# Kernel optimization log

Hardware: AMD Instinct MI355X
Metric: run time of the kernel (lower is better)

Reference implementation:

```python
import jax, jax.numpy as jnp
import numpy as np

EMBED_DIM = 1024
NUM_HEADS = 16
HEAD_DIM = EMBED_DIM // NUM_HEADS
BATCH = 2
SEQ = 2048


def setup_inputs() -> dict:
    key = jax.random.key(0)
    ks = jax.random.split(key, 10)
    s = 1.0 / np.sqrt(EMBED_DIM)
    inp = {
        "query": jax.random.normal(ks[0], (BATCH, SEQ, EMBED_DIM), jnp.float32),
        # Linear weights stored as [in, out] (y = x @ W + b)
        "wq": jax.random.normal(ks[1], (EMBED_DIM, EMBED_DIM), jnp.float32) * s,
        "bq": jnp.zeros((EMBED_DIM,), jnp.float32),
        "wk": jax.random.normal(ks[2], (EMBED_DIM, EMBED_DIM), jnp.float32) * s,
        "bk": jnp.zeros((EMBED_DIM,), jnp.float32),
        "wv": jax.random.normal(ks[3], (EMBED_DIM, EMBED_DIM), jnp.float32) * s,
        "bv": jnp.zeros((EMBED_DIM,), jnp.float32),
        "wo": jax.random.normal(ks[4], (EMBED_DIM, EMBED_DIM), jnp.float32) * s,
        "bo": jnp.zeros((EMBED_DIM,), jnp.float32),
        "temperature": jnp.float32(HEAD_DIM),  # learnable temperature, init = head_dim
    }
    return inp


def reference(query, wq, bq, wk, bk, wv, bv, wo, bo, temperature):
    B, S, E = query.shape
    # self-attention: key = value = query
    Q = (query @ wq + bq).reshape(B, S, NUM_HEADS, HEAD_DIM).transpose(0, 2, 1, 3)
    K = (query @ wk + bk).reshape(B, S, NUM_HEADS, HEAD_DIM).transpose(0, 2, 1, 3)
    V = (query @ wv + bv).reshape(B, S, NUM_HEADS, HEAD_DIM).transpose(0, 2, 1, 3)
    # squared Euclidean distances: ||q||^2 + ||k||^2 - 2<q,k>
    q_sq = jnp.sum(Q * Q, axis=-1, keepdims=True)          # (B,H,Sq,1)
    k_sq = jnp.sum(K * K, axis=-1, keepdims=True)          # (B,H,Sk,1)
    qk = jnp.einsum("bhqd,bhkd->bhqk", Q, K)
    d_sq = jnp.maximum(q_sq + jnp.swapaxes(k_sq, -2, -1) - 2.0 * qk, 0.0)
    attn = jax.nn.softmax(-d_sq / temperature, axis=-1)    # (B,H,Sq,Sk)
    out = jnp.einsum("bhqk,bhkd->bhqd", attn, V)
    out = out.transpose(0, 2, 1, 3).reshape(B, S, E)
    return out @ wo + bo
```

## Files before the change

kernel.cpp:

```cpp
#include <hip/hip_runtime.h>
#include <stdint.h>
#include <stddef.h>


#define LOG2E 1.44269504088896f

typedef __attribute__((ext_vector_type(8))) short bf16x8;
typedef __attribute__((ext_vector_type(4))) float f32x4;
typedef __attribute__((ext_vector_type(4))) unsigned short u16x4;
typedef __attribute__((ext_vector_type(8))) unsigned short u16x8;

__device__ __forceinline__ unsigned short f2b(float f) {
  union { float f; unsigned int u; } x; x.f = f;
  unsigned int u = x.u;
  u += 0x7fffu + ((u >> 16) & 1u);
  return (unsigned short)(u >> 16);
}
__device__ __forceinline__ float b2f(unsigned short s) {
  union { unsigned int u; float f; } x; x.u = ((unsigned int)s) << 16;
  return x.f;
}

#define GLD_LDS(g, l) __builtin_amdgcn_global_load_lds( \
    (const __attribute__((address_space(1))) void*)(g), \
    (__attribute__((address_space(3))) void*)(l), 16, 0, 0)

__global__ void convx_kernel(const float* __restrict__ X, unsigned short* __restrict__ Xb) {
  int i = (blockIdx.x * 256 + threadIdx.x) * 4;
  f32x4 v = *(const f32x4*)&X[i];
  u16x4 o;
  #pragma unroll
  for (int j = 0; j < 4; ++j) o[j] = f2b(v[j]);
  *(u16x4*)&Xb[i] = o;
}

__global__ void transw_kernel(const float* __restrict__ wq, const float* __restrict__ wk,
                              const float* __restrict__ wv, const float* __restrict__ wo,
                              unsigned short* __restrict__ WTqkv, unsigned short* __restrict__ WTo) {
  __shared__ float tile[64][65];
  int z = blockIdx.z;
  const float* src = (z == 0) ? wq : (z == 1) ? wk : (z == 2) ? wv : wo;
  unsigned short* dst = (z < 3) ? (WTqkv + (size_t)z * 1024 * 1024) : WTo;
  int k0 = blockIdx.y * 64, n0 = blockIdx.x * 64;
  int rr = threadIdx.x >> 6, cc = threadIdx.x & 63;
  #pragma unroll
  for (int p = 0; p < 16; ++p) {
    int row = p * 4 + rr;
    tile[row][cc] = src[(size_t)(k0 + row) * 1024 + n0 + cc];
  }
  __syncthreads();
  #pragma unroll
  for (int p = 0; p < 16; ++p) {
    int row = p * 4 + rr;
    dst[(size_t)(n0 + row) * 1024 + k0 + cc] = f2b(tile[cc][row]);
  }
}

__global__ __launch_bounds__(256, 2) void gemm_qkv_kernel(
    const unsigned short* __restrict__ X, const unsigned short* __restrict__ WT,
    const float* __restrict__ bq, const float* __restrict__ bk, const float* __restrict__ bv,
    unsigned short* __restrict__ Qb, unsigned short* __restrict__ Kb,
    unsigned short* __restrict__ VTo) {
  __shared__ unsigned short As[2 * 128 * 32];
  __shared__ unsigned short Bs[2 * 128 * 32];
  const int t = threadIdx.x, w = t >> 6, lane = t & 63;
  const int r = lane & 15, q4 = lane >> 4;
  const int m0 = blockIdx.y * 128, n0 = blockIdx.x * 128;
  const int wr = (w >> 1) * 64, wc = (w & 1) * 64;
  const unsigned short* Xg = X + (size_t)m0 * 1024;
  const unsigned short* Wg = WT + (size_t)n0 * 1024;
  f32x4 acc[4][4] = {};
  for (int k0 = 0; k0 < 1024; k0 += 64) {
    #pragma unroll
    for (int g = 0; g < 4; ++g) {
      int slot = g * 256 + t;
      int kh = slot >> 9, row = (slot >> 2) & 127, ko = (slot & 3) * 8;
      GLD_LDS(Xg + (size_t)row * 1024 + k0 + kh * 32 + ko, &As[(g * 256 + w * 64) * 8]);
      GLD_LDS(Wg + (size_t)row * 1024 + k0 + kh * 32 + ko, &Bs[(g * 256 + w * 64) * 8]);
    }
    __syncthreads();
    #pragma unroll
    for (int kh = 0; kh < 2; ++kh) {
      bf16x8 af[4], bfr[4];
      #pragma unroll
      for (int mf = 0; mf < 4; ++mf)
        af[mf] = *(const bf16x8*)&As[kh * 4096 + (wr + mf * 16 + r) * 32 + q4 * 8];
      #pragma unroll
      for (int nf = 0; nf < 4; ++nf)
        bfr[nf] = *(const bf16x8*)&Bs[kh * 4096 + (wc + nf * 16 + r) * 32 + q4 * 8];
      #pragma unroll
      for (int mf = 0; mf < 4; ++mf)
        #pragma unroll
        for (int nf = 0; nf < 4; ++nf)
          acc[mf][nf] = __builtin_amdgcn_mfma_f32_16x16x32_bf16(af[mf], bfr[nf], acc[mf][nf], 0, 0, 0);
    }
    __syncthreads();
  }
  const int nblk = n0 >> 10;
  if (nblk < 2) {
    const float* bias = (nblk == 0) ? bq : bk;
    unsigned short* OutB = (nblk == 0) ? Qb : Kb;
    const int nc0 = n0 & 1023;
    #pragma unroll
    for (int nf = 0; nf < 4; ++nf) {
      int n = nc0 + wc + nf * 16 + r;
      float bb = bias[n];
      #pragma unroll
      for (int mf = 0; mf < 4; ++mf) {
        int m = m0 + wr + mf * 16 + q4 * 4;
        f32x4 v = acc[mf][nf];
        #pragma unroll
        for (int i = 0; i < 4; ++i)
          OutB[(size_t)(m + i) * 1024 + n] = f2b(v[i] + bb);
      }
    }
  } else {
    const int c0 = n0 - 2048;
    #pragma unroll
    for (int nf = 0; nf < 4; ++nf) {
      int c = c0 + wc + nf * 16 + r;
      float bb = bv[c];
      int h = c >> 6, d = c & 63;
      #pragma unroll
      for (int mf = 0; mf < 4; ++mf) {
        int m = m0 + wr + mf * 16 + q4 * 4;
        int b = m >> 11, s = m & 2047;
        f32x4 v = acc[mf][nf];
        u16x4 pk;
        #pragma unroll
        for (int i = 0; i < 4; ++i) pk[i] = f2b(v[i] + bb);
        *(u16x4*)&VTo[((size_t)((b * 16 + h) * 64 + d)) * 2048 + s] = pk;
      }
    }
  }
}

__global__ void sumsq_kernel(const unsigned short* __restrict__ Qb,
                             const unsigned short* __restrict__ Kb,
                             const float* __restrict__ temp,
                             float* __restrict__ qs2, float* __restrict__ ks2) {
  int idx = blockIdx.x * 256 + threadIdx.x;
  int bh = idx >> 11, s = idx & 2047;
  int b = bh >> 4, h = bh & 15;
  const u16x8* qp = (const u16x8*)(Qb + (size_t)(b * 2048 + s) * 1024 + h * 64);
  const u16x8* kp = (const u16x8*)(Kb + (size_t)(b * 2048 + s) * 1024 + h * 64);
  float scale = LOG2E / temp[0];
  float sq = 0.f, sk = 0.f;
  #pragma unroll
  for (int c = 0; c < 8; ++c) {
    u16x8 vq = qp[c], vk = kp[c];
    #pragma unroll
    for (int j = 0; j < 8; ++j) {
      float q = b2f(vq[j]); sq += q * q;
      float k = b2f(vk[j]); sk += k * k;
    }
  }
  qs2[idx] = sq * scale;
  ks2[idx] = sk * scale;
}

__global__ __launch_bounds__(256, 2) void flash_kernel(
    const unsigned short* __restrict__ Qb, const unsigned short* __restrict__ Kb,
    const unsigned short* __restrict__ VT, const float* __restrict__ qs2,
    const float* __restrict__ ks2, const float* __restrict__ temp,
    unsigned short* __restrict__ AO) {
  __shared__ unsigned short Ks[2][2 * 64 * 32];
  __shared__ unsigned short Vs[2][2 * 64 * 32];
  __shared__ unsigned short Ps[4][32 * 68];
  const int t = threadIdx.x, w = t >> 6, lane = t & 63;
  const int r = lane & 15, q4 = lane >> 4;
  const int bh = blockIdx.y, b = bh >> 4, h = bh & 15;
  const int q0 = blockIdx.x * 128;
  const float cc = 2.0f * LOG2E / temp[0];

  bf16x8 qf[2][2];
  #pragma unroll
  for (int mf = 0; mf < 2; ++mf) {
    int sq = q0 + w * 32 + mf * 16 + r;
    const unsigned short* qp = Qb + (size_t)(b * 2048 + sq) * 1024 + h * 64;
    #pragma unroll
    for (int ks = 0; ks < 2; ++ks) qf[mf][ks] = *(const bf16x8*)(qp + ks * 32 + q4 * 8);
  }
  f32x4 qsv[2];
  #pragma unroll
  for (int mf = 0; mf < 2; ++mf)
    qsv[mf] = *(const f32x4*)&qs2[bh * 2048 + q0 + w * 32 + mf * 16 + q4 * 4];

  f32x4 accO[2][4] = {};
  f32x4 lsum[2] = {};
  bf16x8 ones;
  #pragma unroll
  for (int j = 0; j < 8; ++j) ones[j] = (short)0x3F80;

  const unsigned short* Kg = Kb + ((size_t)b * 2048) * 1024 + h * 64;
  const unsigned short* Vg = VT + ((size_t)bh * 64) * 2048;
  const float* kqb = ks2 + bh * 2048 + r;

  #pragma unroll
  for (int g = 0; g < 2; ++g) {
    int slot = g * 256 + t;
    int half = slot >> 8, key = (slot >> 2) & 63, ko = (slot & 3) * 8;
    GLD_LDS(Kg + (size_t)key * 1024 + half * 32 + ko, &Ks[0][(g * 256 + w * 64) * 8]);
    GLD_LDS(Vg + (size_t)key * 2048 + half * 32 + ko, &Vs[0][(g * 256 + w * 64) * 8]);
  }
  float kq[4];
  #pragma unroll
  for (int nf = 0; nf < 4; ++nf) kq[nf] = kqb[nf * 16];

  #pragma unroll 2
  for (int c = 0; c < 32; ++c) {
    const int buf = c & 1;
    __syncthreads();
    float kqn[4];
    if (c < 31) {
      #pragma unroll
      for (int g = 0; g < 2; ++g) {
        int slot = g * 256 + t;
        int half = slot >> 8, key = (slot >> 2) & 63, ko = (slot & 3) * 8;
        GLD_LDS(Kg + (size_t)((c + 1) * 64 + key) * 1024 + half * 32 + ko,
                &Ks[buf ^ 1][(g * 256 + w * 64) * 8]);
        GLD_LDS(Vg + (size_t)key * 2048 + (c + 1) * 64 + half * 32 + ko,
                &Vs[buf ^ 1][(g * 256 + w * 64) * 8]);
      }
      #pragma unroll
      for (int nf = 0; nf < 4; ++nf) kqn[nf] = kqb[(c + 1) * 64 + nf * 16];
    }

    f32x4 accS[2][4] = {};
    #pragma unroll
    for (int ks = 0; ks < 2; ++ks) {
      #pragma unroll
      for (int nf = 0; nf < 4; ++nf) {
        bf16x8 kf = *(const bf16x8*)&Ks[buf][(ks * 64 + nf * 16 + r) * 32 + q4 * 8];
        accS[0][nf] = __builtin_amdgcn_mfma_f32_16x16x32_bf16(qf[0][ks], kf, accS[0][nf], 0, 0, 0);
        accS[1][nf] = __builtin_amdgcn_mfma_f32_16x16x32_bf16(qf[1][ks], kf, accS[1][nf], 0, 0, 0);
      }
    }
    #pragma unroll
    for (int mf = 0; mf < 2; ++mf) {
      #pragma unroll
      for (int nf = 0; nf < 4; ++nf) {
        #pragma unroll
        for (int i = 0; i < 4; ++i) {
          float u = __builtin_fmaf(cc, accS[mf][nf][i], -kq[nf] - qsv[mf][i]);
          float p = __builtin_amdgcn_exp2f(fminf(u, 0.f));
          union { float f; unsigned int u; } pu; pu.f = p;
          Ps[w][(mf * 16 + q4 * 4 + i) * 68 + nf * 16 + r] = (unsigned short)(pu.u >> 16);
        }
      }
    }
    #pragma unroll
    for (int ks = 0; ks < 2; ++ks) {
      bf16x8 vb[4];
      #pragma unroll
      for (int df = 0; df < 4; ++df)
        vb[df] = *(const bf16x8*)&Vs[buf][(ks * 64 + df * 16 + r) * 32 + q4 * 8];
      #pragma unroll
      for (int mf = 0; mf < 2; ++mf) {
        bf16x8 pa = *(const bf16x8*)&Ps[w][(mf * 16 + r) * 68 + ks * 32 + q4 * 8];
        lsum[mf] = __builtin_amdgcn_mfma_f32_16x16x32_bf16(pa, ones, lsum[mf], 0, 0, 0);
        #pragma unroll
        for (int df = 0; df < 4; ++df)
          accO[mf][df] = __builtin_amdgcn_mfma_f32_16x16x32_bf16(pa, vb[df], accO[mf][df], 0, 0, 0);
      }
    }
    if (c < 31) {
      #pragma unroll
      for (int nf = 0; nf < 4; ++nf) kq[nf] = kqn[nf];
    }
  }
  #pragma unroll
  for (int mf = 0; mf < 2; ++mf) {
    float inv[4];
    #pragma unroll
    for (int i = 0; i < 4; ++i) inv[i] = 1.0f / lsum[mf][i];
    #pragma unroll
    for (int df = 0; df < 4; ++df) {
      int d = df * 16 + r;
      #pragma unroll
      for (int i = 0; i < 4; ++i) {
        int sq = q0 + w * 32 + mf * 16 + q4 * 4 + i;
        AO[(size_t)(b * 2048 + sq) * 1024 + h * 64 + d] = f2b(accO[mf][df][i] * inv[i]);
      }
    }
  }
}

__global__ __launch_bounds__(256, 2) void gemm_out_kernel(
    const unsigned short* __restrict__ A, const unsigned short* __restrict__ WT,
    const float* __restrict__ bo, float* __restrict__ Out) {
  __shared__ unsigned short As[2 * 128 * 32];
  __shared__ unsigned short Bs[2 * 64 * 32];
  const int t = threadIdx.x, w = t >> 6, lane = t & 63;
  const int r = lane & 15, q4 = lane >> 4;
  const int m0 = blockIdx.y * 128, n0 = blockIdx.x * 64;
  const int wr = (w >> 1) * 64, wc = (w & 1) * 32;
  const unsigned short* Ag = A + (size_t)m0 * 1024;
  const unsigned short* Wg = WT + (size_t)n0 * 1024;
  f32x4 acc[4][2] = {};
  for (int k0 = 0; k0 < 1024; k0 += 64) {
    #pragma unroll
    for (int g = 0; g < 4; ++g) {
      int slot = g * 256 + t;
      int kh = slot >> 9, row = (slot >> 2) & 127, ko = (slot & 3) * 8;
      GLD_LDS(Ag + (size_t)row * 1024 + k0 + kh * 32 + ko, &As[(g * 256 + w * 64) * 8]);
    }
    #pragma unroll
    for (int g = 0; g < 2; ++g) {
      int slot = g * 256 + t;
      int kh = slot >> 8, row = (slot >> 2) & 63, ko = (slot & 3) * 8;
      GLD_LDS(Wg + (size_t)row * 1024 + k0 + kh * 32 + ko, &Bs[(g * 256 + w * 64) * 8]);
    }
    __syncthreads();
    #pragma unroll
    for (int kh = 0; kh < 2; ++kh) {
      bf16x8 af[4], bfr[2];
      #pragma unroll
      for (int mf = 0; mf < 4; ++mf)
        af[mf] = *(const bf16x8*)&As[kh * 4096 + (wr + mf * 16 + r) * 32 + q4 * 8];
      #pragma unroll
      for (int nf = 0; nf < 2; ++nf)
        bfr[nf] = *(const bf16x8*)&Bs[kh * 2048 + (wc + nf * 16 + r) * 32 + q4 * 8];
      #pragma unroll
      for (int mf = 0; mf < 4; ++mf)
        #pragma unroll
        for (int nf = 0; nf < 2; ++nf)
          acc[mf][nf] = __builtin_amdgcn_mfma_f32_16x16x32_bf16(af[mf], bfr[nf], acc[mf][nf], 0, 0, 0);
    }
    __syncthreads();
  }
  #pragma unroll
  for (int nf = 0; nf < 2; ++nf) {
    int n = n0 + wc + nf * 16 + r;
    float bb = bo[n];
    #pragma unroll
    for (int mf = 0; mf < 4; ++mf) {
      int m = m0 + wr + mf * 16 + q4 * 4;
      f32x4 v = acc[mf][nf];
      #pragma unroll
      for (int i = 0; i < 4; ++i)
        Out[(size_t)(m + i) * 1024 + n] = v[i] + bb;
    }
  }
}

extern "C" void kernel_launch(void* const* d_in, const int* in_sizes, int n_in,
                              void* d_out, int out_size, void* d_ws, size_t ws_size,
                              hipStream_t stream) {
  const float* X    = (const float*)d_in[0];
  const float* wq   = (const float*)d_in[1];
  const float* bq   = (const float*)d_in[2];
  const float* wk   = (const float*)d_in[3];
  const float* bk   = (const float*)d_in[4];
  const float* wv   = (const float*)d_in[5];
  const float* bv   = (const float*)d_in[6];
  const float* wo   = (const float*)d_in[7];
  const float* bo   = (const float*)d_in[8];
  const float* temp = (const float*)d_in[9];
  float* Out = (float*)d_out;

  char* ws = (char*)d_ws;
  unsigned short* Xb    = (unsigned short*)ws; ws += (size_t)4096 * 1024 * 2;
  unsigned short* WTqkv = (unsigned short*)ws; ws += (size_t)3072 * 1024 * 2;
  unsigned short* WTo   = (unsigned short*)ws; ws += (size_t)1024 * 1024 * 2;
  unsigned short* Qb    = (unsigned short*)ws; ws += (size_t)4096 * 1024 * 2;
  unsigned short* Kb    = (unsigned short*)ws; ws += (size_t)4096 * 1024 * 2;
  unsigned short* VT    = (unsigned short*)ws; ws += (size_t)4096 * 1024 * 2;
  unsigned short* AO    = (unsigned short*)ws; ws += (size_t)4096 * 1024 * 2;
  float* qs2 = (float*)ws; ws += (size_t)65536 * 4;
  float* ks2 = (float*)ws; ws += (size_t)65536 * 4;

  convx_kernel<<<4096, 256, 0, stream>>>(X, Xb);
  transw_kernel<<<dim3(16, 16, 4), 256, 0, stream>>>(wq, wk, wv, wo, WTqkv, WTo);
  gemm_qkv_kernel<<<dim3(24, 32), 256, 0, stream>>>(Xb, WTqkv, bq, bk, bv, Qb, Kb, VT);
  sumsq_kernel<<<256, 256, 0, stream>>>(Qb, Kb, temp, qs2, ks2);
  flash_kernel<<<dim3(16, 32), 256, 0, stream>>>(Qb, Kb, VT, qs2, ks2, temp, AO);
  gemm_out_kernel<<<dim3(16, 32), 256, 0, stream>>>(AO, WTo, bo, Out);
}
```

Measured before the change: 209.8 us.

## Fuse prep kernels, fold sum-of-squares into QKV GEMM, keep P in registers

Merges the X conversion and weight transpose into one launch, and computes the per-head squared norms of Q and K inside the QKV GEMM epilogue using shuffle reductions, which removes the separate sumsq kernel and its re-read of Q and K. The flash kernel now computes S transposed, so the exponentiated probabilities land directly in MFMA A-operand layout. This drops the LDS round trip through Ps. V tiles are stored in LDS with an XOR swizzle and read as two 4-element halves, and the QKV GEMM launch bounds are raised to 3 blocks per SM. The changes add epilogue work and register pressure in the GEMM in exchange for fewer launches and less memory traffic.

```diff
diff --git a/kernel.cpp b/kernel.cpp
--- a/kernel.cpp
+++ b/kernel.cpp
@@ -6,9 +6,9 @@
 #define LOG2E 1.44269504088896f
 
 typedef __attribute__((ext_vector_type(8))) short bf16x8;
+typedef __attribute__((ext_vector_type(4))) short bf16x4;
 typedef __attribute__((ext_vector_type(4))) float f32x4;
 typedef __attribute__((ext_vector_type(4))) unsigned short u16x4;
-typedef __attribute__((ext_vector_type(8))) unsigned short u16x8;
 
 __device__ __forceinline__ unsigned short f2b(float f) {
   union { float f; unsigned int u; } x; x.f = f;
@@ -20,25 +20,34 @@
   union { unsigned int u; float f; } x; x.u = ((unsigned int)s) << 16;
   return x.f;
 }
+__device__ __forceinline__ unsigned int fbits(float f) {
+  union { float f; unsigned int u; } x; x.f = f; return x.u;
+}
 
 #define GLD_LDS(g, l) __builtin_amdgcn_global_load_lds( \
     (const __attribute__((address_space(1))) void*)(g), \
     (__attribute__((address_space(3))) void*)(l), 16, 0, 0)
 
-__global__ void convx_kernel(const float* __restrict__ X, unsigned short* __restrict__ Xb) {
-  int i = (blockIdx.x * 256 + threadIdx.x) * 4;
-  f32x4 v = *(const f32x4*)&X[i];
-  u16x4 o;
-  #pragma unroll
-  for (int j = 0; j < 4; ++j) o[j] = f2b(v[j]);
-  *(u16x4*)&Xb[i] = o;
-}
-
-__global__ void transw_kernel(const float* __restrict__ wq, const float* __restrict__ wk,
-                              const float* __restrict__ wv, const float* __restrict__ wo,
-                              unsigned short* __restrict__ WTqkv, unsigned short* __restrict__ WTo) {
+__global__ void prep_kernel(const float* __restrict__ X,
+                            const float* __restrict__ wq, const float* __restrict__ wk,
+                            const float* __restrict__ wv, const float* __restrict__ wo,
+                            unsigned short* __restrict__ Xb,
+                            unsigned short* __restrict__ WTqkv, unsigned short* __restrict__ WTo) {
+  int z = blockIdx.z;
+  if (z == 4) {
+    size_t base = ((size_t)(blockIdx.y * 16 + blockIdx.x)) * 16384;
+    #pragma unroll
+    for (int j = 0; j < 16; ++j) {
+      size_t i = base + (size_t)(j * 256 + threadIdx.x) * 4;
+      f32x4 v = *(const f32x4*)&X[i];
+      u16x4 o;
+      #pragma unroll
+      for (int k = 0; k < 4; ++k) o[k] = f2b(v[k]);
+      *(u16x4*)&Xb[i] = o;
+    }
+    return;
+  }
   __shared__ float tile[64][65];
-  int z = blockIdx.z;
   const float* src = (z == 0) ? wq : (z == 1) ? wk : (z == 2) ? wv : wo;
   unsigned short* dst = (z < 3) ? (WTqkv + (size_t)z * 1024 * 1024) : WTo;
   int k0 = blockIdx.y * 64, n0 = blockIdx.x * 64;
@@ -56,11 +65,11 @@
   }
 }
 
-__global__ __launch_bounds__(256, 2) void gemm_qkv_kernel(
+__global__ __launch_bounds__(256, 3) void gemm_qkv_kernel(
     const unsigned short* __restrict__ X, const unsigned short* __restrict__ WT,
     const float* __restrict__ bq, const float* __restrict__ bk, const float* __restrict__ bv,
     unsigned short* __restrict__ Qb, unsigned short* __restrict__ Kb,
-    unsigned short* __restrict__ VTo) {
+    unsigned short* __restrict__ VTo, float* __restrict__ qs2, float* __restrict__ ks2) {
   __shared__ unsigned short As[2 * 128 * 32];
   __shared__ unsigned short Bs[2 * 128 * 32];
   const int t = threadIdx.x, w = t >> 6, lane = t & 63;
@@ -100,7 +109,9 @@
   if (nblk < 2) {
     const float* bias = (nblk == 0) ? bq : bk;
     unsigned short* OutB = (nblk == 0) ? Qb : Kb;
+    float* S2 = (nblk == 0) ? qs2 : ks2;
     const int nc0 = n0 & 1023;
+    float s2a[4][4] = {};
     #pragma unroll
     for (int nf = 0; nf < 4; ++nf) {
       int n = nc0 + wc + nf * 16 + r;
@@ -110,8 +121,34 @@
         int m = m0 + wr + mf * 16 + q4 * 4;
         f32x4 v = acc[mf][nf];
         #pragma unroll
+        for (int i = 0; i < 4; ++i) {
+          unsigned short os = f2b(v[i] + bb);
+          OutB[(size_t)(m + i) * 1024 + n] = os;
+          float xb = b2f(os);
+          s2a[mf][i] += xb * xb;
+        }
+      }
+    }
+    #pragma unroll
+    for (int mf = 0; mf < 4; ++mf)
+      #pragma unroll
+      for (int i = 0; i < 4; ++i) {
+        float v = s2a[mf][i];
+        v += __shfl_xor(v, 1, 64);
+        v += __shfl_xor(v, 2, 64);
+        v += __shfl_xor(v, 4, 64);
+        v += __shfl_xor(v, 8, 64);
+        s2a[mf][i] = v;
+      }
+    if (r == 0) {
+      int hh = (nc0 + wc) >> 6;
+      #pragma unroll
+      for (int mf = 0; mf < 4; ++mf) {
+        int m = m0 + wr + mf * 16 + q4 * 4;
+        int bb2 = m >> 11, ss = m & 2047;
+        #pragma unroll
         for (int i = 0; i < 4; ++i)
-          OutB[(size_t)(m + i) * 1024 + n] = f2b(v[i] + bb);
+          S2[(size_t)(bb2 * 16 + hh) * 2048 + ss + i] = s2a[mf][i];
       }
     }
   } else {
@@ -135,43 +172,19 @@
   }
 }
 
-__global__ void sumsq_kernel(const unsigned short* __restrict__ Qb,
-                             const unsigned short* __restrict__ Kb,
-                             const float* __restrict__ temp,
-                             float* __restrict__ qs2, float* __restrict__ ks2) {
-  int idx = blockIdx.x * 256 + threadIdx.x;
-  int bh = idx >> 11, s = idx & 2047;
-  int b = bh >> 4, h = bh & 15;
-  const u16x8* qp = (const u16x8*)(Qb + (size_t)(b * 2048 + s) * 1024 + h * 64);
-  const u16x8* kp = (const u16x8*)(Kb + (size_t)(b * 2048 + s) * 1024 + h * 64);
-  float scale = LOG2E / temp[0];
-  float sq = 0.f, sk = 0.f;
-  #pragma unroll
-  for (int c = 0; c < 8; ++c) {
-    u16x8 vq = qp[c], vk = kp[c];
-    #pragma unroll
-    for (int j = 0; j < 8; ++j) {
-      float q = b2f(vq[j]); sq += q * q;
-      float k = b2f(vk[j]); sk += k * k;
-    }
-  }
-  qs2[idx] = sq * scale;
-  ks2[idx] = sk * scale;
-}
-
 __global__ __launch_bounds__(256, 2) void flash_kernel(
     const unsigned short* __restrict__ Qb, const unsigned short* __restrict__ Kb,
     const unsigned short* __restrict__ VT, const float* __restrict__ qs2,
     const float* __restrict__ ks2, const float* __restrict__ temp,
     unsigned short* __restrict__ AO) {
-  __shared__ unsigned short Ks[2][2 * 64 * 32];
-  __shared__ unsigned short Vs[2][2 * 64 * 32];
-  __shared__ unsigned short Ps[4][32 * 68];
+  __shared__ unsigned short Ks[2][64 * 64];
+  __shared__ unsigned short Vs[2][64 * 64];
   const int t = threadIdx.x, w = t >> 6, lane = t & 63;
   const int r = lane & 15, q4 = lane >> 4;
   const int bh = blockIdx.y, b = bh >> 4, h = bh & 15;
   const int q0 = blockIdx.x * 128;
-  const float cc = 2.0f * LOG2E / temp[0];
+  const float scale = LOG2E / temp[0];
+  const float cc = 2.0f * scale;
 
   bf16x8 qf[2][2];
   #pragma unroll
@@ -181,10 +194,10 @@
     #pragma unroll
     for (int ks = 0; ks < 2; ++ks) qf[mf][ks] = *(const bf16x8*)(qp + ks * 32 + q4 * 8);
   }
-  f32x4 qsv[2];
+  float qs_s[2];
   #pragma unroll
   for (int mf = 0; mf < 2; ++mf)
-    qsv[mf] = *(const f32x4*)&qs2[bh * 2048 + q0 + w * 32 + mf * 16 + q4 * 4];
+    qs_s[mf] = scale * qs2[bh * 2048 + q0 + w * 32 + mf * 16 + r];
 
   f32x4 accO[2][4] = {};
   f32x4 lsum[2] = {};
@@ -194,79 +207,104 @@
 
   const unsigned short* Kg = Kb + ((size_t)b * 2048) * 1024 + h * 64;
   const unsigned short* Vg = VT + ((size_t)bh * 64) * 2048;
-  const float* kqb = ks2 + bh * 2048 + r;
+  const float* kqb = ks2 + bh * 2048;
 
   #pragma unroll
   for (int g = 0; g < 2; ++g) {
     int slot = g * 256 + t;
-    int half = slot >> 8, key = (slot >> 2) & 63, ko = (slot & 3) * 8;
-    GLD_LDS(Kg + (size_t)key * 1024 + half * 32 + ko, &Ks[0][(g * 256 + w * 64) * 8]);
-    GLD_LDS(Vg + (size_t)key * 2048 + half * 32 + ko, &Vs[0][(g * 256 + w * 64) * 8]);
-  }
-  float kq[4];
-  #pragma unroll
-  for (int nf = 0; nf < 4; ++nf) kq[nf] = kqb[nf * 16];
+    int khalf = slot >> 8, key = (slot >> 2) & 63, ko = (slot & 3) * 8;
+    GLD_LDS(Kg + (size_t)key * 1024 + khalf * 32 + ko, &Ks[0][slot * 8]);
+    int dd = slot >> 3, gg = (slot & 7) ^ (dd & 7);
+    GLD_LDS(Vg + (size_t)dd * 2048 + gg * 8, &Vs[0][slot * 8]);
+  }
+  f32x4 kq[4];
+  #pragma unroll
+  for (int kfm = 0; kfm < 4; ++kfm) {
+    f32x4 raw = *(const f32x4*)&kqb[kfm * 16 + q4 * 4];
+    #pragma unroll
+    for (int i = 0; i < 4; ++i) kq[kfm][i] = scale * raw[i];
+  }
 
   #pragma unroll 2
   for (int c = 0; c < 32; ++c) {
     const int buf = c & 1;
     __syncthreads();
-    float kqn[4];
+    f32x4 kqn[4];
     if (c < 31) {
       #pragma unroll
       for (int g = 0; g < 2; ++g) {
         int slot = g * 256 + t;
-        int half = slot >> 8, key = (slot >> 2) & 63, ko = (slot & 3) * 8;
-        GLD_LDS(Kg + (size_t)((c + 1) * 64 + key) * 1024 + half * 32 + ko,
-                &Ks[buf ^ 1][(g * 256 + w * 64) * 8]);
-        GLD_LDS(Vg + (size_t)key * 2048 + (c + 1) * 64 + half * 32 + ko,
-                &Vs[buf ^ 1][(g * 256 + w * 64) * 8]);
-      }
-      #pragma unroll
-      for (int nf = 0; nf < 4; ++nf) kqn[nf] = kqb[(c + 1) * 64 + nf * 16];
-    }
-
-    f32x4 accS[2][4] = {};
+        int khalf = slot >> 8, key = (slot >> 2) & 63, ko = (slot & 3) * 8;
+        GLD_LDS(Kg + (size_t)((c + 1) * 64 + key) * 1024 + khalf * 32 + ko,
+                &Ks[buf ^ 1][slot * 8]);
+        int dd = slot >> 3, gg = (slot & 7) ^ (dd & 7);
+        GLD_LDS(Vg + (size_t)dd * 2048 + (c + 1) * 64 + gg * 8,
+                &Vs[buf ^ 1][slot * 8]);
+      }
+      #pragma unroll
+      for (int kfm = 0; kfm < 4; ++kfm) {
+        f32x4 raw = *(const f32x4*)&kqb[(c + 1) * 64 + kfm * 16 + q4 * 4];
+        #pragma unroll
+        for (int i = 0; i < 4; ++i) kqn[kfm][i] = scale * raw[i];
+      }
+    }
+
+    f32x4 accST[4][2] = {};
     #pragma unroll
     for (int ks = 0; ks < 2; ++ks) {
       #pragma unroll
-      for (int nf = 0; nf < 4; ++nf) {
-        bf16x8 kf = *(const bf16x8*)&Ks[buf][(ks * 64 + nf * 16 + r) * 32 + q4 * 8];
-        accS[0][nf] = __builtin_amdgcn_mfma_f32_16x16x32_bf16(qf[0][ks], kf, accS[0][nf], 0, 0, 0);
-        accS[1][nf] = __builtin_amdgcn_mfma_f32_16x16x32_bf16(qf[1][ks], kf, accS[1][nf], 0, 0, 0);
-      }
-    }
-    #pragma unroll
-    for (int mf = 0; mf < 2; ++mf) {
-      #pragma unroll
-      for (int nf = 0; nf < 4; ++nf) {
-        #pragma unroll
-        for (int i = 0; i < 4; ++i) {
-          float u = __builtin_fmaf(cc, accS[mf][nf][i], -kq[nf] - qsv[mf][i]);
-          float p = __builtin_amdgcn_exp2f(fminf(u, 0.f));
-          union { float f; unsigned int u; } pu; pu.f = p;
-          Ps[w][(mf * 16 + q4 * 4 + i) * 68 + nf * 16 + r] = (unsigned short)(pu.u >> 16);
+      for (int kfm = 0; kfm < 4; ++kfm) {
+        bf16x8 ka = *(const bf16x8*)&Ks[buf][(ks * 64 + kfm * 16 + r) * 32 + q4 * 8];
+        accST[kfm][0] = __builtin_amdgcn_mfma_f32_16x16x32_bf16(ka, qf[0][ks], accST[kfm][0], 0, 0, 0);
+        accST[kfm][1] = __builtin_amdgcn_mfma_f32_16x16x32_bf16(ka, qf[1][ks], accST[kfm][1], 0, 0, 0);
+      }
+    }
+
+    bf16x8 pf[2][2];
+    #pragma unroll
+    for (int cb = 0; cb < 2; ++cb) {
+      #pragma unroll
+      for (int mf = 0; mf < 2; ++mf) {
+        unsigned int dw[4];
+        #pragma unroll
+        for (int half = 0; half < 2; ++half) {
+          int kfm = cb * 2 + half;
+          float pp[4];
+          #pragma unroll
+          for (int i = 0; i < 4; ++i) {
+            float u = __builtin_fmaf(cc, accST[kfm][mf][i], -(kq[kfm][i] + qs_s[mf]));
+            pp[i] = __builtin_amdgcn_exp2f(fminf(u, 0.f));
+          }
+          dw[half * 2 + 0] = (fbits(pp[0]) >> 16) | (fbits(pp[1]) & 0xFFFF0000u);
+          dw[half * 2 + 1] = (fbits(pp[2]) >> 16) | (fbits(pp[3]) & 0xFFFF0000u);
         }
-      }
-    }
-    #pragma unroll
-    for (int ks = 0; ks < 2; ++ks) {
-      bf16x8 vb[4];
-      #pragma unroll
-      for (int df = 0; df < 4; ++df)
-        vb[df] = *(const bf16x8*)&Vs[buf][(ks * 64 + df * 16 + r) * 32 + q4 * 8];
-      #pragma unroll
-      for (int mf = 0; mf < 2; ++mf) {
-        bf16x8 pa = *(const bf16x8*)&Ps[w][(mf * 16 + r) * 68 + ks * 32 + q4 * 8];
-        lsum[mf] = __builtin_amdgcn_mfma_f32_16x16x32_bf16(pa, ones, lsum[mf], 0, 0, 0);
-        #pragma unroll
-        for (int df = 0; df < 4; ++df)
-          accO[mf][df] = __builtin_amdgcn_mfma_f32_16x16x32_bf16(pa, vb[df], accO[mf][df], 0, 0, 0);
+        union { unsigned int d[4]; bf16x8 v; } cv;
+        cv.d[0] = dw[0]; cv.d[1] = dw[1]; cv.d[2] = dw[2]; cv.d[3] = dw[3];
+        pf[cb][mf] = cv.v;
+      }
+    }
+
+    #pragma unroll
+    for (int cb = 0; cb < 2; ++cb) {
+      #pragma unroll
+      for (int mf = 0; mf < 2; ++mf)
+        lsum[mf] = __builtin_amdgcn_mfma_f32_16x16x32_bf16(pf[cb][mf], ones, lsum[mf], 0, 0, 0);
+      #pragma unroll
+      for (int df = 0; df < 4; ++df) {
+        int dloc = df * 16 + r;
+        int e0 = (cb * 4 + (q4 >> 1)) ^ (r & 7);
+        int e1 = (cb * 4 + 2 + (q4 >> 1)) ^ (r & 7);
+        bf16x4 v0 = *(const bf16x4*)&Vs[buf][dloc * 64 + e0 * 8 + (q4 & 1) * 4];
+        bf16x4 v1 = *(const bf16x4*)&Vs[buf][dloc * 64 + e1 * 8 + (q4 & 1) * 4];
+        bf16x8 vb = __builtin_shufflevector(v0, v1, 0, 1, 2, 3, 4, 5, 6, 7);
+        #pragma unroll
+        for (int mf = 0; mf < 2; ++mf)
+          accO[mf][df] = __builtin_amdgcn_mfma_f32_16x16x32_bf16(pf[cb][mf], vb, accO[mf][df], 0, 0, 0);
       }
     }
     if (c < 31) {
       #pragma unroll
-      for (int nf = 0; nf < 4; ++nf) kq[nf] = kqn[nf];
+      for (int kfm = 0; kfm < 4; ++kfm) kq[kfm] = kqn[kfm];
     }
   }
   #pragma unroll
@@ -370,10 +408,8 @@
   float* qs2 = (float*)ws; ws += (size_t)65536 * 4;
   float* ks2 = (float*)ws; ws += (size_t)65536 * 4;
 
-  convx_kernel<<<4096, 256, 0, stream>>>(X, Xb);
-  transw_kernel<<<dim3(16, 16, 4), 256, 0, stream>>>(wq, wk, wv, wo, WTqkv, WTo);
-  gemm_qkv_kernel<<<dim3(24, 32), 256, 0, stream>>>(Xb, WTqkv, bq, bk, bv, Qb, Kb, VT);
-  sumsq_kernel<<<256, 256, 0, stream>>>(Qb, Kb, temp, qs2, ks2);
+  prep_kernel<<<dim3(16, 16, 5), 256, 0, stream>>>(X, wq, wk, wv, wo, Xb, WTqkv, WTo);
+  gemm_qkv_kernel<<<dim3(24, 32), 256, 0, stream>>>(Xb, WTqkv, bq, bk, bv, Qb, Kb, VT, qs2, ks2);
   flash_kernel<<<dim3(16, 32), 256, 0, stream>>>(Qb, Kb, VT, qs2, ks2, temp, AO);
   gemm_out_kernel<<<dim3(16, 32), 256, 0, stream>>>(AO, WTo, bo, Out);
 }
```

Result: no change. 208.5 us (-0.6%).
